# Optimization experiments

Measured on AMD Instinct MI355X. Metric: run time of the kernel, lower is better.

Reference implementation:

```python
import jax, jax.numpy as jnp
import numpy as np

L, N_ATOMS, N_PROBES, E, H = 3, 20000, 100000, 400000, 128
CUTOFF, STEP, EDGE_SIZE = 4.0, 0.25, 16
LOG2 = float(np.log(2.0))

def ssp(x):
    # ShiftedSoftplus: softplus(x) - log(2)
    return jax.nn.softplus(x) - LOG2

def mlp(x, W1, b1, W2, b2):
    return ssp(x @ W1 + b1) @ W2 + b2

def setup_inputs() -> dict:
    key = jax.random.key(0)
    ks = iter(jax.random.split(key, 32))
    def nrm(shape, s=0.05):
        return jax.random.normal(next(ks), shape, dtype=jnp.float32) * s
    inp = {
        'atom_rep': nrm((L, N_ATOMS, H), 1.0),
        'dist': jax.random.uniform(next(ks), (E, 1), dtype=jnp.float32) * CUTOFF,
    }
    pshapes = {
        'msg_We1': (L, EDGE_SIZE, H), 'msg_be1': (L, H),
        'msg_We2': (L, H, H), 'msg_be2': (L, H),
        'msg_Wn1': (L, 2 * H, H), 'msg_bn1': (L, H),
        'msg_Wn2': (L, H, H), 'msg_bn2': (L, H),
        'gate_W1': (L, H, H), 'gate_b1': (L, H),
        'gate_W2': (L, H, H), 'gate_b2': (L, H),
        'trans_W1': (L, H, H), 'trans_b1': (L, H),
        'trans_W2': (L, H, H), 'trans_b2': (L, H),
        'readout_W1': (H, H), 'readout_b1': (H,),
        'readout_W2': (H, 1), 'readout_b2': (1,),
    }
    for name, shp in pshapes.items():
        inp[name] = nrm(shp)
    senders = jax.random.randint(next(ks), (E, 1), 0, N_ATOMS)
    receivers = jax.random.randint(next(ks), (E, 1), 0, N_PROBES)
    inp['probe_edges'] = jnp.concatenate([senders, receivers], axis=1).astype(jnp.int32)
    return inp

def reference(atom_rep, dist, msg_We1, msg_be1, msg_We2, msg_be2, msg_Wn1, msg_bn1, msg_Wn2, msg_bn2, gate_W1, gate_b1, gate_W2, gate_b2, trans_W1, trans_b1, trans_W2, trans_b2, readout_W1, readout_b1, readout_W2, readout_b2, probe_edges):
    # gaussian_expansion of edge distances: [E, EDGE_SIZE]
    mu = jnp.arange(0.0, CUTOFF, STEP, dtype=jnp.float32)
    edge_state = jnp.exp(-((dist - mu) ** 2) / (2.0 * STEP * STEP))
    # SchnetMessageFunction soft cutoff on raw distance: [E, 1]
    soft_cut = 1.0 - jax.nn.sigmoid(5.0 * (dist - (CUTOFF - 1.5)))
    snd = probe_edges[:, 0]  # atom senders
    rcv = probe_edges[:, 1]  # probe receivers
    probe_state0 = jnp.zeros((N_PROBES, H), dtype=jnp.float32)

    def step(probe_state, layer):
        (nodes_l, We1, be1, We2, be2, Wn1, bn1, Wn2, bn2,
         gW1, gb1, gW2, gb2, tW1, tb1, tW2, tb2) = layer
        # edge filter gates [E, H]
        gates_msg = mlp(edge_state, We1, be1, We2, be2) * soft_cut
        # include_receiver=True with receiver_nodes=probe_state: concat sender atom / receiver probe
        nodes = jnp.concatenate([nodes_l[snd], probe_state[rcv]], axis=1)  # [E, 2H]
        messages = mlp(nodes, Wn1, bn1, Wn2, bn2) * gates_msg  # [E, H]
        msgsum = jax.ops.segment_sum(messages, rcv, num_segments=N_PROBES)  # [P, H]
        g = jax.nn.sigmoid(mlp(probe_state, gW1, gb1, gW2, gb2))
        new_state = probe_state * g + (1.0 - g) * mlp(msgsum, tW1, tb1, tW2, tb2)
        return new_state, None

    xs = (atom_rep, msg_We1, msg_be1, msg_We2, msg_be2, msg_Wn1, msg_bn1,
          msg_Wn2, msg_bn2, gate_W1, gate_b1, gate_W2, gate_b2,
          trans_W1, trans_b1, trans_W2, trans_b2)
    probe_state, _ = jax.lax.scan(step, probe_state0, xs)
    out = mlp(probe_state, readout_W1, readout_b1, readout_W2, readout_b2)[:, 0]  # [P]
    return out
```

## Files before the change

kernel.cpp:

```cpp
#include <hip/hip_runtime.h>

#define NLAYER 3
#define NATOM 20000
#define NPROBE 100000
#define NEDGE 400000
#define HD 128
#define NBIN 2048
#define CUTOFFF 4.0f
#define PLANE 16384
#define MT 64
#define NT 512
#define NSBLK ((NPROBE + 255) / 256)

typedef unsigned int u32;
typedef unsigned short u16;
typedef __attribute__((ext_vector_type(8))) short bf16x8;
typedef __attribute__((ext_vector_type(4))) float f32x4;

__device__ __forceinline__ float sspf(float x) {
    float e = __builtin_amdgcn_exp2f(fminf(x, 80.f) * 1.44269504088896341f);
    return 0.69314718055994531f * (__builtin_amdgcn_logf(1.f + e) - 1.f);
}
__device__ __forceinline__ float sigf(float x) {
    return 1.f / (1.f + __builtin_amdgcn_exp2f(-x * 1.44269504088896341f));
}
__device__ __forceinline__ void atomic_add_f(float* p, float v) {
    __hip_atomic_fetch_add(p, v, __ATOMIC_RELAXED, __HIP_MEMORY_SCOPE_AGENT);
}
__device__ __forceinline__ u32 atomic_add_u(u32* p, u32 v) {
    return __hip_atomic_fetch_add(p, v, __ATOMIC_RELAXED, __HIP_MEMORY_SCOPE_AGENT);
}
__device__ __forceinline__ u32 f2u(float f) { union { float f; u32 u; } x; x.f = f; return x.u; }
__device__ __forceinline__ float u2f(u32 u) { union { float f; u32 u; } x; x.u = u; return x.f; }
__device__ __forceinline__ u16 bf16rn(float f) {
    u32 u = f2u(f);
    u32 r = u + 0x7fffu + ((u >> 16) & 1u);
    return (u16)(r >> 16);
}
__device__ __forceinline__ void split_pair(float x, float y, u32& hi, u32& lo) {
    u32 ux = f2u(x);
    u32 hx = (ux + 0x7fffu + ((ux >> 16) & 1u)) & 0xffff0000u;
    float lxf = x - u2f(hx);
    u32 uy = f2u(y);
    u32 hy = (uy + 0x7fffu + ((uy >> 16) & 1u)) & 0xffff0000u;
    float lyf = y - u2f(hy);
    hi = (hx >> 16) | hy;
    lo = (f2u(lxf) >> 16) | (f2u(lyf) & 0xffff0000u);
}

__device__ __forceinline__ void bar_lds() {
    asm volatile("s_waitcnt lgkmcnt(0)" ::: "memory");
    __builtin_amdgcn_s_barrier();
}

__device__ __forceinline__ void load_bfrags(const u16* __restrict__ Wb, int lane, int wid,
                                            bf16x8 Bh[4], bf16x8 Bl[4]) {
    const bf16x8* Bhp = (const bf16x8*)Wb;
    const bf16x8* Blp = (const bf16x8*)(Wb + PLANE);
#pragma unroll
    for (int c = 0; c < 4; ++c) {
        Bh[c] = Bhp[(size_t)(c * 8 + wid) * 64 + lane];
        Bl[c] = Blp[(size_t)(c * 8 + wid) * 64 + lane];
    }
}

__device__ __forceinline__ void mma_slice_pre(const u16* __restrict__ ldsH,
                                              const u16* __restrict__ ldsL,
                                              int lane, const bf16x8 Bh[4], const bf16x8 Bl[4],
                                              f32x4 acc[4]) {
    int l15 = lane & 15, kq = lane >> 4;
#pragma unroll
    for (int m = 0; m < 4; ++m) {
        int row = m * 16 + l15;
        int s = row & 7;
        const u16* hp = ldsH + row * 128;
        const u16* lp = ldsL + row * 128;
#pragma unroll
        for (int c = 0; c < 4; ++c) {
            int off = ((c * 4 + kq) ^ s) << 3;
            bf16x8 Ah = *(const bf16x8*)(hp + off);
            bf16x8 Al = *(const bf16x8*)(lp + off);
            acc[m] = __builtin_amdgcn_mfma_f32_16x16x32_bf16(Ah, Bh[c], acc[m], 0, 0, 0);
            acc[m] = __builtin_amdgcn_mfma_f32_16x16x32_bf16(Al, Bh[c], acc[m], 0, 0, 0);
            acc[m] = __builtin_amdgcn_mfma_f32_16x16x32_bf16(Ah, Bl[c], acc[m], 0, 0, 0);
        }
    }
}

__device__ __forceinline__ void mma_slice(const u16* __restrict__ ldsH,
                                          const u16* __restrict__ ldsL,
                                          int lane, int wid,
                                          const u16* __restrict__ Wb,
                                          f32x4 acc[4]) {
    bf16x8 Bh[4], Bl[4];
    load_bfrags(Wb, lane, wid, Bh, Bl);
    mma_slice_pre(ldsH, ldsL, lane, Bh, Bl, acc);
}

__device__ __forceinline__ void pack_store(const float* v, int row, int q,
                                           u16* ldsH, u16* ldsL) {
    int s = row & 7;
#pragma unroll
    for (int h = 0; h < 2; ++h) {
        u32 hv[4], lv[4];
#pragma unroll
        for (int k = 0; k < 4; ++k)
            split_pair(v[8 * h + 2 * k], v[8 * h + 2 * k + 1], hv[k], lv[k]);
        int gc = q * 2 + h;
        int off = row * 128 + ((gc ^ s) << 3);
        *(uint4*)(ldsH + off) = make_uint4(hv[0], hv[1], hv[2], hv[3]);
        *(uint4*)(ldsL + off) = make_uint4(lv[0], lv[1], lv[2], lv[3]);
    }
}

__device__ __forceinline__ void gather_rows(const float* __restrict__ A, int M,
                                            int m0, int t, float* v) {
    int r = t >> 3, q = t & 7;
    int row = m0 + r;
    bool ok = row < M;
    const float4* src = (const float4*)(A + (size_t)row * HD + q * 16);
#pragma unroll
    for (int j = 0; j < 4; ++j) {
        float4 x = ok ? src[j] : make_float4(0.f, 0.f, 0.f, 0.f);
        v[4 * j] = x.x; v[4 * j + 1] = x.y; v[4 * j + 2] = x.z; v[4 * j + 3] = x.w;
    }
}
__device__ __forceinline__ void zero_rows(float* A, int M, int m0, int t) {
    int r = t >> 3, q = t & 7;
    int row = m0 + r;
    if (row < M) {
        float4* dst = (float4*)(A + (size_t)row * HD + q * 16);
        float4 z = make_float4(0.f, 0.f, 0.f, 0.f);
#pragma unroll
        for (int j = 0; j < 4; ++j) dst[j] = z;
    }
}
__device__ __forceinline__ void stage_split(const float* __restrict__ A, int M,
                                            int m0, int t, u16* ldsH, u16* ldsL) {
    float v[16];
    gather_rows(A, M, m0, t, v);
    pack_store(v, t >> 3, t & 7, ldsH, ldsL);
}

__device__ __forceinline__ void h_store(u16* ldsH, u16* ldsL, int wid, int lane,
                                        const f32x4 acc[4], const float* __restrict__ bias) {
    int l15 = lane & 15, lq = lane >> 4;
    int col = wid * 16 + l15;
    float bb = bias[col];
    int gc = col >> 3, wg = col & 7;
#pragma unroll
    for (int m = 0; m < 4; ++m) {
#pragma unroll
        for (int r = 0; r < 4; ++r) {
            int row = m * 16 + lq * 4 + r;
            float h = sspf(acc[m][r] + bb);
            u32 u = f2u(h);
            u32 hh = (u + 0x7fffu + ((u >> 16) & 1u)) & 0xffff0000u;
            float lf = h - u2f(hh);
            int off = row * 128 + ((gc ^ (row & 7)) << 3) + wg;
            ldsH[off] = (u16)(hh >> 16);
            ldsL[off] = (u16)(f2u(lf) >> 16);
        }
    }
}
__device__ __forceinline__ void v_store(u16* ldsH, u16* ldsL, int wid, int lane,
                                        int m, int r, float val) {
    int l15 = lane & 15, lq = lane >> 4;
    int col = wid * 16 + l15;
    int gc = col >> 3, wg = col & 7;
    int row = m * 16 + lq * 4 + r;
    u32 u = f2u(val);
    u32 hh = (u + 0x7fffu + ((u >> 16) & 1u)) & 0xffff0000u;
    float lf = val - u2f(hh);
    int off = row * 128 + ((gc ^ (row & 7)) << 3) + wg;
    ldsH[off] = (u16)(hh >> 16);
    ldsL[off] = (u16)(f2u(lf) >> 16);
}

__global__ void convert_w_k(const float* __restrict__ Wn1, const float* __restrict__ Wn2,
                            const float* __restrict__ gW1, const float* __restrict__ gW2,
                            const float* __restrict__ tW1, const float* __restrict__ tW2,
                            const float* __restrict__ rW1, u16* __restrict__ Wb) {
    int m = blockIdx.x;
    const float* src;
    if (m < 6)       src = Wn1 + (size_t)(m >> 1) * (2 * HD * HD) + (size_t)(m & 1) * (HD * HD);
    else if (m < 9)  src = Wn2 + (size_t)(m - 6) * HD * HD;
    else if (m < 12) src = gW1 + (size_t)(m - 9) * HD * HD;
    else if (m < 15) src = gW2 + (size_t)(m - 12) * HD * HD;
    else if (m < 18) src = tW1 + (size_t)(m - 15) * HD * HD;
    else if (m < 21) src = tW2 + (size_t)(m - 18) * HD * HD;
    else             src = rW1;
    int t = threadIdx.x;
    int lane = t & 63, nn = t >> 6;
    u16* dh = Wb + (size_t)m * (2 * PLANE);
    u16* dl = dh + PLANE;
    for (int c = 0; c < 4; ++c) {
        for (int hh = 0; hh < 2; ++hh) {
            int n = nn + hh * 4;
            int col = n * 16 + (lane & 15);
            int k0 = c * 32 + (lane >> 4) * 8;
            u32 hv[4], lv[4];
#pragma unroll
            for (int jj = 0; jj < 4; ++jj) {
                float wA = src[(size_t)(k0 + 2 * jj) * HD + col];
                float wB = src[(size_t)(k0 + 2 * jj + 1) * HD + col];
                u16 ha = bf16rn(wA), hb = bf16rn(wB);
                u16 la = bf16rn(wA - u2f((u32)ha << 16));
                u16 lb = bf16rn(wB - u2f((u32)hb << 16));
                hv[jj] = (u32)ha | ((u32)hb << 16);
                lv[jj] = (u32)la | ((u32)lb << 16);
            }
            size_t off = ((size_t)(c * 8 + n) * 64 + lane) * 8;
            *(uint4*)(dh + off) = make_uint4(hv[0], hv[1], hv[2], hv[3]);
            *(uint4*)(dl + off) = make_uint4(lv[0], lv[1], lv[2], lv[3]);
        }
    }
}

__global__ void gate_table_k(const float* __restrict__ We1, const float* __restrict__ be1,
                             const float* __restrict__ We2, const float* __restrict__ be2,
                             float2* __restrict__ gt2) {
    int row = blockIdx.x;
    int l = row / (NBIN + 1);
    int i = row % (NBIN + 1);
    int j = threadIdx.x;
    float d = (CUTOFFF / NBIN) * (float)i;
    __shared__ float h1[HD];
    const float* w1 = We1 + (size_t)l * 16 * HD;
    float acc = be1[l * HD + j];
#pragma unroll
    for (int k = 0; k < 16; ++k) {
        float dd = d - 0.25f * (float)k;
        float es = __builtin_amdgcn_exp2f(-dd * dd * 8.0f * 1.44269504088896341f);
        acc = fmaf(es, w1[k * HD + j], acc);
    }
    h1[j] = sspf(acc);
    __syncthreads();
    const float* w2 = We2 + (size_t)l * HD * HD;
    float acc2 = be2[l * HD + j];
    for (int k = 0; k < HD; ++k) acc2 = fmaf(h1[k], w2[k * HD + j], acc2);
    float sc = 1.f - sigf(5.f * (d - (CUTOFFF - 1.5f)));
    float val = acc2 * sc;
    float2* base = gt2 + (size_t)l * NBIN * HD;
    if (i < NBIN) base[(size_t)i * HD + j].x = val;
    if (i > 0)    base[(size_t)(i - 1) * HD + j].y = val;
}

__global__ void gate0_k(const float* __restrict__ gW2, const float* __restrict__ gb1,
                        const float* __restrict__ gb2, float* __restrict__ g0v) {
    int j = threadIdx.x;
    __shared__ float h[HD];
    h[j] = sspf(gb1[j]);
    __syncthreads();
    float acc = gb2[j];
    for (int k = 0; k < HD; ++k) acc = fmaf(h[k], gW2[k * HD + j], acc);
    g0v[j] = sigf(acc);
}

__global__ __launch_bounds__(256) void hist_k(const int* __restrict__ pe, u32* __restrict__ cnt) {
    int e = blockIdx.x * 256 + threadIdx.x;
    if (e < NEDGE) atomic_add_u(&cnt[pe[2 * e + 1]], 1u);
}

__global__ __launch_bounds__(256) void bsum_k(const u32* __restrict__ cnt, u32* __restrict__ bsum) {
    int i = blockIdx.x * 256 + threadIdx.x;
    int v = (i < NPROBE) ? (int)cnt[i] : 0;
#pragma unroll
    for (int d = 1; d < 64; d <<= 1) v += __shfl_xor(v, d);
    __shared__ int wsum[4];
    if ((threadIdx.x & 63) == 0) wsum[threadIdx.x >> 6] = v;
    __syncthreads();
    if (threadIdx.x == 0) bsum[blockIdx.x] = (u32)(wsum[0] + wsum[1] + wsum[2] + wsum[3]);
}

__global__ __launch_bounds__(512) void bscan_k(u32* __restrict__ bsum) {
    __shared__ u32 s[512];
    int t = threadIdx.x;
    u32 v = (t < NSBLK) ? bsum[t] : 0u;
    s[t] = v;
    __syncthreads();
    for (int d = 1; d < 512; d <<= 1) {
        u32 x = (t >= d) ? s[t - d] : 0u;
        __syncthreads();
        s[t] += x;
        __syncthreads();
    }
    if (t < NSBLK) bsum[t] = s[t] - v;
}

__global__ __launch_bounds__(256) void cur_k(const u32* __restrict__ cnt,
                                             const u32* __restrict__ bsum, u32* __restrict__ cur) {
    __shared__ u32 s[256];
    int b = blockIdx.x, t = threadIdx.x;
    int i = b * 256 + t;
    u32 v = (i < NPROBE) ? cnt[i] : 0u;
    s[t] = v;
    __syncthreads();
    for (int d = 1; d < 256; d <<= 1) {
        u32 x = (t >= d) ? s[t - d] : 0u;
        __syncthreads();
        s[t] += x;
        __syncthreads();
    }
    if (i < NPROBE) cur[i] = bsum[b] + s[t] - v;
}

__global__ __launch_bounds__(256) void scatter_k(const int* __restrict__ pe,
                                                 u32* __restrict__ cur, u32* __restrict__ eord) {
    int e = blockIdx.x * 256 + threadIdx.x;
    if (e < NEDGE) {
        u32 pos = atomic_add_u(&cur[pe[2 * e + 1]], 1u);
        eord[pos] = (u32)e;
    }
}

#define ABLK 313
__global__ __launch_bounds__(NT, 4) void gemm_atoms_k(const float* __restrict__ atom_rep,
                                                      const u16* __restrict__ Wb,
                                                      const float* __restrict__ bn1,
                                                      float* __restrict__ Xab) {
    __shared__ u16 ldsH[MT * 128];
    __shared__ u16 ldsL[MT * 128];
    int l = blockIdx.x / ABLK;
    int mb = blockIdx.x % ABLK;
    const float* A = atom_rep + (size_t)l * NATOM * HD;
    const u16* W = Wb + (size_t)(2 * l) * 2 * PLANE;
    float* outp = Xab + (size_t)l * NATOM * HD;
    int m0 = mb * MT, t = threadIdx.x;
    stage_split(A, NATOM, m0, t, ldsH, ldsL);
    bar_lds();
    int lane = t & 63, wid = t >> 6;
    int l15 = lane & 15, lq = lane >> 4;
    int col = wid * 16 + l15;
    f32x4 acc[4] = {};
    mma_slice(ldsH, ldsL, lane, wid, W, acc);
    float bv = bn1[l * HD + col];
#pragma unroll
    for (int m = 0; m < 4; ++m) {
#pragma unroll
        for (int r = 0; r < 4; ++r) {
            int row = m0 + m * 16 + lq * 4 + r;
            if (row < NATOM) outp[(size_t)row * HD + col] = acc[m][r] + bv;
        }
    }
}

__device__ __forceinline__ int rho(int r) {
    return ((r >> 2) & 3) * 16 + ((r >> 4) << 2) + (r & 3);
}

__device__ __forceinline__ void gather_edge(
        int e0, int t, const float* __restrict__ Xab, const float* __restrict__ Xp,
        const int* __restrict__ pe, const u32* __restrict__ eord,
        const float* __restrict__ dist,
        u32* mix_s, float* fr_s, float* sum) {
    int r = t >> 3, q = t & 7;
    int e = (int)eord[e0 + r];
    int snd = pe[2 * e], rcv = pe[2 * e + 1];
    if (q == 0) {
        float x = dist[e] * ((float)NBIN / CUTOFFF);
        int i = (int)x;
        i = i < (NBIN - 1) ? i : (NBIN - 1);
        fr_s[r] = x - (float)i;
        mix_s[r] = ((u32)rcv << 11) | (u32)i;
    }
    const float4* xa = (const float4*)(Xab + (size_t)snd * HD + q * 16);
    const float4* xp = Xp ? (const float4*)(Xp + (size_t)rcv * HD + q * 16) : nullptr;
#pragma unroll
    for (int j = 0; j < 4; ++j) {
        float4 va = xa[j];
        if (xp) {
            float4 vp = xp[j];
            va.x += vp.x; va.y += vp.y; va.z += vp.z; va.w += vp.w;
        }
        sum[4 * j] = va.x; sum[4 * j + 1] = va.y;
        sum[4 * j + 2] = va.z; sum[4 * j + 3] = va.w;
    }
}

__device__ __forceinline__ void pack_ssp_edge(const float* v, int r, int q,
                                              u16* ldsH, u16* ldsL) {
    float h[16];
#pragma unroll
    for (int k = 0; k < 16; ++k) h[k] = sspf(v[k]);
    pack_store(h, rho(r), q, ldsH, ldsL);
}

__device__ __forceinline__ void edge_out(const f32x4 acc[4], const u32* mix_s,
        const float* fr_s, const float2* __restrict__ gt2,
        float bb, int col, int lq, float* __restrict__ msgsum) {
    float carry = 0.f;
    int rcc = -1;
#pragma unroll
    for (int m = 3; m >= 0; --m) {
        int ebase = lq * 16 + m * 4;
        float vals[4];
        int rc[4];
#pragma unroll
        for (int r = 0; r < 4; ++r) {
            u32 mx = mix_s[ebase + r];
            rc[r] = (int)(mx >> 11);
            float2 g2 = gt2[(size_t)(mx & 2047u) * HD + col];
            vals[r] = (acc[m][r] + bb) * fmaf(g2.y - g2.x, fr_s[ebase + r], g2.x);
        }
        if (rcc == rc[3]) vals[3] += carry;
        else if (rcc >= 0) atomic_add_f(msgsum + (size_t)rcc * HD + col, carry);
#pragma unroll
        for (int r = 3; r >= 1; --r) {
            if (rc[r] == rc[r - 1]) vals[r - 1] += vals[r];
            else atomic_add_f(msgsum + (size_t)rc[r] * HD + col, vals[r]);
        }
        carry = vals[0];
        rcc = rc[0];
    }
    atomic_add_f(msgsum + (size_t)rcc * HD + col, carry);
}

__global__ __launch_bounds__(NT, 4) void edge_msg_k(
        const float* __restrict__ Xab, const float* __restrict__ Xp,
        const u16* __restrict__ W2b, const float* __restrict__ bn2,
        const float2* __restrict__ gt2, const float* __restrict__ dist,
        const int* __restrict__ pe, const u32* __restrict__ eord,
        float* __restrict__ msgsum) {
    __shared__ u16 ldsH[2][MT * 128];
    __shared__ u16 ldsL[2][MT * 128];
    __shared__ u32 mix_s[2][MT];
    __shared__ float fr_s[2][MT];
    int t = threadIdx.x;
    int lane = t & 63, wid = t >> 6;
    int l15 = lane & 15, lq = lane >> 4;
    int col = wid * 16 + l15;
    int e0 = blockIdx.x * (2 * MT);

    bf16x8 Bh[4], Bl[4];
    load_bfrags(W2b, lane, wid, Bh, Bl);
    float bb = bn2[col];

    float s0[16], s1[16];
    gather_edge(e0, t, Xab, Xp, pe, eord, dist, mix_s[0], fr_s[0], s0);
    gather_edge(e0 + MT, t, Xab, Xp, pe, eord, dist, mix_s[1], fr_s[1], s1);
    pack_ssp_edge(s0, t >> 3, t & 7, ldsH[0], ldsL[0]);
    bar_lds();

    f32x4 acc0[4] = {};
    mma_slice_pre(ldsH[0], ldsL[0], lane, Bh, Bl, acc0);
    pack_ssp_edge(s1, t >> 3, t & 7, ldsH[1], ldsL[1]);
    edge_out(acc0, mix_s[0], fr_s[0], gt2, bb, col, lq, msgsum);
    bar_lds();

    f32x4 acc1[4] = {};
    mma_slice_pre(ldsH[1], ldsL[1], lane, Bh, Bl, acc1);
    edge_out(acc1, mix_s[1], fr_s[1], gt2, bb, col, lq, msgsum);
}

__global__ __launch_bounds__(NT, 4) void probe_update_k(
        const float* ps, const float* msgsum, float* msgzero,
        const u16* __restrict__ gW1b, const float* __restrict__ gb1,
        const u16* __restrict__ gW2b, const float* __restrict__ gb2,
        const u16* __restrict__ tW1b, const float* __restrict__ tb1,
        const u16* __restrict__ tW2b, const float* __restrict__ tb2,
        const u16* __restrict__ W3b,
        const u16* __restrict__ rW1b, const float* __restrict__ rb1,
        const float* __restrict__ rW2, const float* __restrict__ rb2,
        const float* __restrict__ g0v,
        float* psout, float* __restrict__ xpout, float* __restrict__ outp) {
    __shared__ u16 ldsH[2][MT * 128];
    __shared__ u16 ldsL[2][MT * 128];
    __shared__ float parts[MT][9];
    int m0 = blockIdx.x * MT, t = threadIdx.x;
    int lane = t & 63, wid = t >> 6;
    int l15 = lane & 15, lq = lane >> 4;
    int col = wid * 16 + l15;

    f32x4 g[4] = {};
    f32x4 tv[4] = {};
    int vbuf;

    if (!g0v) {
        float sp[16], sm[16];
        gather_rows(ps, NPROBE, m0, t, sp);
        gather_rows(msgsum, NPROBE, m0, t, sm);
        pack_store(sp, t >> 3, t & 7, ldsH[0], ldsL[0]);
        bar_lds();
        pack_store(sm, t >> 3, t & 7, ldsH[1], ldsL[1]);
        if (msgzero) zero_rows(msgzero, NPROBE, m0, t);
        mma_slice(ldsH[0], ldsL[0], lane, wid, gW1b, g);
        bar_lds();
        h_store(ldsH[0], ldsL[0], wid, lane, g, gb1);
        mma_slice(ldsH[1], ldsL[1], lane, wid, tW1b, tv);
        bar_lds();
#pragma unroll
        for (int m = 0; m < 4; ++m) g[m] = (f32x4){0.f, 0.f, 0.f, 0.f};
        mma_slice(ldsH[0], ldsL[0], lane, wid, gW2b, g);
        float gb2v = gb2[col];
#pragma unroll
        for (int m = 0; m < 4; ++m)
#pragma unroll
            for (int r = 0; r < 4; ++r) g[m][r] = sigf(g[m][r] + gb2v);
        h_store(ldsH[1], ldsL[1], wid, lane, tv, tb1);
        bar_lds();
#pragma unroll
        for (int m = 0; m < 4; ++m) tv[m] = (f32x4){0.f, 0.f, 0.f, 0.f};
        mma_slice(ldsH[1], ldsL[1], lane, wid, tW2b, tv);
        vbuf = 0;
    } else {
        float sm[16];
        gather_rows(msgsum, NPROBE, m0, t, sm);
        pack_store(sm, t >> 3, t & 7, ldsH[0], ldsL[0]);
        if (msgzero) zero_rows(msgzero, NPROBE, m0, t);
        bar_lds();
        mma_slice(ldsH[0], ldsL[0], lane, wid, tW1b, tv);
        bar_lds();
        h_store(ldsH[0], ldsL[0], wid, lane, tv, tb1);
        bar_lds();
#pragma unroll
        for (int m = 0; m < 4; ++m) tv[m] = (f32x4){0.f, 0.f, 0.f, 0.f};
        mma_slice(ldsH[0], ldsL[0], lane, wid, tW2b, tv);
        float gv = g0v[col];
#pragma unroll
        for (int m = 0; m < 4; ++m)
#pragma unroll
            for (int r = 0; r < 4; ++r) g[m][r] = gv;
        vbuf = 1;
    }

    float tb2v = tb2[col];
#pragma unroll
    for (int m = 0; m < 4; ++m) {
#pragma unroll
        for (int r = 0; r < 4; ++r) {
            int row = m0 + m * 16 + lq * 4 + r;
            float val = 0.f;
            if (row < NPROBE) {
                size_t idx = (size_t)row * HD + col;
                float tval = tv[m][r] + tb2v;
                float pv = g0v ? 0.f : ps[idx];
                val = fmaf(pv - tval, g[m][r], tval);
                if (!rW1b) psout[idx] = val;
            }
            v_store(ldsH[vbuf], ldsL[vbuf], wid, lane, m, r, val);
        }
    }
    bar_lds();

    if (W3b) {
        f32x4 a[4] = {};
        mma_slice(ldsH[vbuf], ldsL[vbuf], lane, wid, W3b, a);
#pragma unroll
        for (int m = 0; m < 4; ++m)
#pragma unroll
            for (int r = 0; r < 4; ++r) {
                int row = m0 + m * 16 + lq * 4 + r;
                if (row < NPROBE) xpout[(size_t)row * HD + col] = a[m][r];
            }
    } else if (rW1b) {
        f32x4 a[4] = {};
        mma_slice(ldsH[vbuf], ldsL[vbuf], lane, wid, rW1b, a);
        float rb1v = rb1[col], w2v = rW2[col];
#pragma unroll
        for (int m = 0; m < 4; ++m)
#pragma unroll
            for (int r = 0; r < 4; ++r) {
                float p = sspf(a[m][r] + rb1v) * w2v;
                p += __shfl_xor(p, 1, 16);
                p += __shfl_xor(p, 2, 16);
                p += __shfl_xor(p, 4, 16);
                p += __shfl_xor(p, 8, 16);
                if (l15 == 0) parts[m * 16 + lq * 4 + r][wid] = p;
            }
        bar_lds();
        if (t < MT) {
            int row = m0 + t;
            if (row < NPROBE) {
                float s = rb2[0];
#pragma unroll
                for (int w = 0; w < 8; ++w) s += parts[t][w];
                outp[row] = s;
            }
        }
    }
}

extern "C" void kernel_launch(void* const* d_in, const int* in_sizes, int n_in,
                              void* d_out, int out_size, void* d_ws, size_t ws_size,
                              hipStream_t stream) {
    const float* atom_rep = (const float*)d_in[0];
    const float* dist     = (const float*)d_in[1];
    const float* We1 = (const float*)d_in[2];
    const float* be1 = (const float*)d_in[3];
    const float* We2 = (const float*)d_in[4];
    const float* be2 = (const float*)d_in[5];
    const float* Wn1 = (const float*)d_in[6];
    const float* bn1 = (const float*)d_in[7];
    const float* Wn2 = (const float*)d_in[8];
    const float* bn2 = (const float*)d_in[9];
    const float* gW1 = (const float*)d_in[10];
    const float* gb1 = (const float*)d_in[11];
    const float* gW2 = (const float*)d_in[12];
    const float* gb2 = (const float*)d_in[13];
    const float* tW1 = (const float*)d_in[14];
    const float* tb1 = (const float*)d_in[15];
    const float* tW2 = (const float*)d_in[16];
    const float* tb2 = (const float*)d_in[17];
    const float* rW1 = (const float*)d_in[18];
    const float* rb1 = (const float*)d_in[19];
    const float* rW2 = (const float*)d_in[20];
    const float* rb2 = (const float*)d_in[21];
    const int*   pe  = (const int*)d_in[22];
    float* out = (float*)d_out;

    float* ws = (float*)d_ws;
    float* ps     = ws;
    float* msgsum = ps + 12800000u;
    float* Xp     = msgsum + 12800000u;
    float* Xab    = Xp + 12800000u;
    float2* gt2   = (float2*)(Xab + 7680000u);
    float* g0v    = (float*)(gt2 + (size_t)NLAYER * NBIN * HD);
    u16*   Wb     = (u16*)(g0v + 128);
    u32*   cnt    = (u32*)(Wb + 22 * 2 * PLANE);
    u32*   bsum   = cnt + NPROBE;
    u32*   cur    = bsum + 512;
    u32*   eord   = cur + NPROBE;

    const int PBLK = (NPROBE + MT - 1) / MT;
    const int EBLK = NEDGE / (2 * MT);
    const int TBLK = (NEDGE + 255) / 256;

    hipMemsetAsync(cnt, 0, (size_t)NPROBE * 4, stream);
    hipMemsetAsync(msgsum, 0, 12800000ull * 4, stream);
    convert_w_k<<<22, 256, 0, stream>>>(Wn1, Wn2, gW1, gW2, tW1, tW2, rW1, Wb);
    gate_table_k<<<NLAYER * (NBIN + 1), HD, 0, stream>>>(We1, be1, We2, be2, gt2);
    gate0_k<<<1, HD, 0, stream>>>(gW2, gb1, gb2, g0v);
    hist_k<<<TBLK, 256, 0, stream>>>(pe, cnt);
    bsum_k<<<NSBLK, 256, 0, stream>>>(cnt, bsum);
    bscan_k<<<1, 512, 0, stream>>>(bsum);
    cur_k<<<NSBLK, 256, 0, stream>>>(cnt, bsum, cur);
    scatter_k<<<TBLK, 256, 0, stream>>>(pe, cur, eord);
    gemm_atoms_k<<<NLAYER * ABLK, NT, 0, stream>>>(atom_rep, Wb, bn1, Xab);

    for (int l = 0; l < NLAYER; ++l) {
        edge_msg_k<<<EBLK, NT, 0, stream>>>(Xab + (size_t)l * NATOM * HD,
                                            (l == 0) ? nullptr : Xp,
                                            Wb + (size_t)(6 + l) * 2 * PLANE,
                                            bn2 + l * HD,
                                            gt2 + (size_t)l * NBIN * HD,
                                            dist, pe, eord, msgsum);
        const u16* W3  = (l < NLAYER - 1) ? Wb + (size_t)(2 * (l + 1) + 1) * 2 * PLANE : nullptr;
        const u16* RW1 = (l == NLAYER - 1) ? Wb + (size_t)21 * 2 * PLANE : nullptr;
        float* mz = (l < NLAYER - 1) ? msgsum : nullptr;
        probe_update_k<<<PBLK, NT, 0, stream>>>(ps, msgsum, mz,
                                                Wb + (size_t)(9 + l) * 2 * PLANE, gb1 + l * HD,
                                                Wb + (size_t)(12 + l) * 2 * PLANE, gb2 + l * HD,
                                                Wb + (size_t)(15 + l) * 2 * PLANE, tb1 + l * HD,
                                                Wb + (size_t)(18 + l) * 2 * PLANE, tb2 + l * HD,
                                                W3, RW1, rb1, rW2, rb2,
                                                (l == 0) ? g0v : nullptr,
                                                ps, Xp, out);
    }
}
```

Before: 706.8 us.

## Halve LDS footprint, raise occupancy, and swizzle edge blocks across XCDs

The edge message kernel now processes one 64-edge tile per block with single-buffered LDS instead of two tiles double-buffered. The probe update kernel is restructured to reuse a single LDS buffer, running the gate MLP and then the transform MLP sequentially. Launch bounds are raised to 8 waves-per-EU hint to allow more resident blocks. A block-index swizzle assigns contiguous edge ranges to each of the 8 XCDs for L2 locality of the receiver-sorted atomics. The cost is losing the intra-block overlap of gather/pack with MMA, plus possible register pressure or spills under the tighter bounds.

```diff
diff --git a/kernel.cpp b/kernel.cpp
--- a/kernel.cpp
+++ b/kernel.cpp
@@ -51,6 +51,12 @@
 __device__ __forceinline__ void bar_lds() {
     asm volatile("s_waitcnt lgkmcnt(0)" ::: "memory");
     __builtin_amdgcn_s_barrier();
+}
+
+__device__ __forceinline__ int bswz(int b, int nb) {
+    int q = nb >> 3, r = nb & 7;
+    int x = b & 7, o = b >> 3;
+    return (x < r ? x * (q + 1) : r * (q + 1) + (x - r) * q) + o;
 }
 
 __device__ __forceinline__ void load_bfrags(const u16* __restrict__ Wb, int lane, int wid,
@@ -315,7 +321,7 @@
 }
 
 #define ABLK 313
-__global__ __launch_bounds__(NT, 4) void gemm_atoms_k(const float* __restrict__ atom_rep,
+__global__ __launch_bounds__(NT, 8) void gemm_atoms_k(const float* __restrict__ atom_rep,
                                                       const u16* __restrict__ Wb,
                                                       const float* __restrict__ bn1,
                                                       float* __restrict__ Xab) {
@@ -416,44 +422,38 @@
     atomic_add_f(msgsum + (size_t)rcc * HD + col, carry);
 }
 
-__global__ __launch_bounds__(NT, 4) void edge_msg_k(
+__global__ __launch_bounds__(NT, 8) void edge_msg_k(
         const float* __restrict__ Xab, const float* __restrict__ Xp,
         const u16* __restrict__ W2b, const float* __restrict__ bn2,
         const float2* __restrict__ gt2, const float* __restrict__ dist,
         const int* __restrict__ pe, const u32* __restrict__ eord,
         float* __restrict__ msgsum) {
-    __shared__ u16 ldsH[2][MT * 128];
-    __shared__ u16 ldsL[2][MT * 128];
-    __shared__ u32 mix_s[2][MT];
-    __shared__ float fr_s[2][MT];
+    __shared__ u16 ldsH[MT * 128];
+    __shared__ u16 ldsL[MT * 128];
+    __shared__ u32 mix_s[MT];
+    __shared__ float fr_s[MT];
     int t = threadIdx.x;
     int lane = t & 63, wid = t >> 6;
     int l15 = lane & 15, lq = lane >> 4;
     int col = wid * 16 + l15;
-    int e0 = blockIdx.x * (2 * MT);
+    const int nb = NEDGE / MT;
+    int e0 = bswz(blockIdx.x, nb) * MT;
 
     bf16x8 Bh[4], Bl[4];
     load_bfrags(W2b, lane, wid, Bh, Bl);
     float bb = bn2[col];
 
-    float s0[16], s1[16];
-    gather_edge(e0, t, Xab, Xp, pe, eord, dist, mix_s[0], fr_s[0], s0);
-    gather_edge(e0 + MT, t, Xab, Xp, pe, eord, dist, mix_s[1], fr_s[1], s1);
-    pack_ssp_edge(s0, t >> 3, t & 7, ldsH[0], ldsL[0]);
+    float s0[16];
+    gather_edge(e0, t, Xab, Xp, pe, eord, dist, mix_s, fr_s, s0);
+    pack_ssp_edge(s0, t >> 3, t & 7, ldsH, ldsL);
     bar_lds();
 
-    f32x4 acc0[4] = {};
-    mma_slice_pre(ldsH[0], ldsL[0], lane, Bh, Bl, acc0);
-    pack_ssp_edge(s1, t >> 3, t & 7, ldsH[1], ldsL[1]);
-    edge_out(acc0, mix_s[0], fr_s[0], gt2, bb, col, lq, msgsum);
-    bar_lds();
-
-    f32x4 acc1[4] = {};
-    mma_slice_pre(ldsH[1], ldsL[1], lane, Bh, Bl, acc1);
-    edge_out(acc1, mix_s[1], fr_s[1], gt2, bb, col, lq, msgsum);
-}
-
-__global__ __launch_bounds__(NT, 4) void probe_update_k(
+    f32x4 acc[4] = {};
+    mma_slice_pre(ldsH, ldsL, lane, Bh, Bl, acc);
+    edge_out(acc, mix_s, fr_s, gt2, bb, col, lq, msgsum);
+}
+
+__global__ __launch_bounds__(NT, 8) void probe_update_k(
         const float* ps, const float* msgsum, float* msgzero,
         const u16* __restrict__ gW1b, const float* __restrict__ gb1,
         const u16* __restrict__ gW2b, const float* __restrict__ gb2,
@@ -464,8 +464,8 @@
         const float* __restrict__ rW2, const float* __restrict__ rb2,
         const float* __restrict__ g0v,
         float* psout, float* __restrict__ xpout, float* __restrict__ outp) {
-    __shared__ u16 ldsH[2][MT * 128];
-    __shared__ u16 ldsL[2][MT * 128];
+    __shared__ u16 ldsH[MT * 128];
+    __shared__ u16 ldsL[MT * 128];
     __shared__ float parts[MT][9];
     int m0 = blockIdx.x * MT, t = threadIdx.x;
     int lane = t & 63, wid = t >> 6;
@@ -474,55 +474,47 @@
 
     f32x4 g[4] = {};
     f32x4 tv[4] = {};
-    int vbuf;
+
+    float sm[16];
+    gather_rows(msgsum, NPROBE, m0, t, sm);
 
     if (!g0v) {
-        float sp[16], sm[16];
-        gather_rows(ps, NPROBE, m0, t, sp);
-        gather_rows(msgsum, NPROBE, m0, t, sm);
-        pack_store(sp, t >> 3, t & 7, ldsH[0], ldsL[0]);
+        stage_split(ps, NPROBE, m0, t, ldsH, ldsL);
         bar_lds();
-        pack_store(sm, t >> 3, t & 7, ldsH[1], ldsL[1]);
-        if (msgzero) zero_rows(msgzero, NPROBE, m0, t);
-        mma_slice(ldsH[0], ldsL[0], lane, wid, gW1b, g);
+        mma_slice(ldsH, ldsL, lane, wid, gW1b, g);
         bar_lds();
-        h_store(ldsH[0], ldsL[0], wid, lane, g, gb1);
-        mma_slice(ldsH[1], ldsL[1], lane, wid, tW1b, tv);
+        h_store(ldsH, ldsL, wid, lane, g, gb1);
         bar_lds();
 #pragma unroll
         for (int m = 0; m < 4; ++m) g[m] = (f32x4){0.f, 0.f, 0.f, 0.f};
-        mma_slice(ldsH[0], ldsL[0], lane, wid, gW2b, g);
+        mma_slice(ldsH, ldsL, lane, wid, gW2b, g);
         float gb2v = gb2[col];
 #pragma unroll
         for (int m = 0; m < 4; ++m)
 #pragma unroll
             for (int r = 0; r < 4; ++r) g[m][r] = sigf(g[m][r] + gb2v);
-        h_store(ldsH[1], ldsL[1], wid, lane, tv, tb1);
         bar_lds();
-#pragma unroll
-        for (int m = 0; m < 4; ++m) tv[m] = (f32x4){0.f, 0.f, 0.f, 0.f};
-        mma_slice(ldsH[1], ldsL[1], lane, wid, tW2b, tv);
-        vbuf = 0;
     } else {
-        float sm[16];
-        gather_rows(msgsum, NPROBE, m0, t, sm);
-        pack_store(sm, t >> 3, t & 7, ldsH[0], ldsL[0]);
-        if (msgzero) zero_rows(msgzero, NPROBE, m0, t);
-        bar_lds();
-        mma_slice(ldsH[0], ldsL[0], lane, wid, tW1b, tv);
-        bar_lds();
-        h_store(ldsH[0], ldsL[0], wid, lane, tv, tb1);
-        bar_lds();
-#pragma unroll
-        for (int m = 0; m < 4; ++m) tv[m] = (f32x4){0.f, 0.f, 0.f, 0.f};
-        mma_slice(ldsH[0], ldsL[0], lane, wid, tW2b, tv);
         float gv = g0v[col];
 #pragma unroll
         for (int m = 0; m < 4; ++m)
 #pragma unroll
             for (int r = 0; r < 4; ++r) g[m][r] = gv;
-        vbuf = 1;
-    }
+    }
+
+    pack_store(sm, t >> 3, t & 7, ldsH, ldsL);
+    if (msgzero) zero_rows(msgzero, NPROBE, m0, t);
+    bar_lds();
+    mma_slice(ldsH, ldsL, lane, wid, tW1b, tv);
+    bar_lds();
+    h_store(ldsH, ldsL, wid, lane, tv, tb1);
+    bar_lds();
+#pragma unroll
+    for (int m = 0; m < 4; ++m) tv[m] = (f32x4){0.f, 0.f, 0.f, 0.f};
+    mma_slice(ldsH, ldsL, lane, wid, tW2b, tv);
+
+    bool proj = (W3b != nullptr) || (rW1b != nullptr);
+    if (proj) bar_lds();
 
     float tb2v = tb2[col];
 #pragma unroll
@@ -538,14 +530,15 @@
                 val = fmaf(pv - tval, g[m][r], tval);
                 if (!rW1b) psout[idx] = val;
             }
-            v_store(ldsH[vbuf], ldsL[vbuf], wid, lane, m, r, val);
-        }
-    }
+            if (proj) v_store(ldsH, ldsL, wid, lane, m, r, val);
+        }
+    }
+    if (!proj) return;
     bar_lds();
 
     if (W3b) {
         f32x4 a[4] = {};
-        mma_slice(ldsH[vbuf], ldsL[vbuf], lane, wid, W3b, a);
+        mma_slice(ldsH, ldsL, lane, wid, W3b, a);
 #pragma unroll
         for (int m = 0; m < 4; ++m)
 #pragma unroll
@@ -553,9 +546,9 @@
                 int row = m0 + m * 16 + lq * 4 + r;
                 if (row < NPROBE) xpout[(size_t)row * HD + col] = a[m][r];
             }
-    } else if (rW1b) {
+    } else {
         f32x4 a[4] = {};
-        mma_slice(ldsH[vbuf], ldsL[vbuf], lane, wid, rW1b, a);
+        mma_slice(ldsH, ldsL, lane, wid, rW1b, a);
         float rb1v = rb1[col], w2v = rW2[col];
 #pragma unroll
         for (int m = 0; m < 4; ++m)
@@ -623,7 +616,7 @@
     u32*   eord   = cur + NPROBE;
 
     const int PBLK = (NPROBE + MT - 1) / MT;
-    const int EBLK = NEDGE / (2 * MT);
+    const int EBLK = NEDGE / MT;
     const int TBLK = (NEDGE + 255) / 256;
 
     hipMemsetAsync(cnt, 0, (size_t)NPROBE * 4, stream);
```

Measured after the change: 1.440 ms. 104% more time.
